# Kernel optimization log

Hardware: AMD Instinct MI355X
Metric: run time of the kernel (lower is better)

Reference implementation:

```python
import jax, jax.numpy as jnp
import numpy as np

B, S, M = 128, 4096, 20
LOG_2PI = float(np.log(2.0 * np.pi))


def setup_inputs() -> dict:
    key = jax.random.key(0)
    k1, k2, k3, k4, k5 = jax.random.split(key, 5)
    xs = jax.random.normal(k1, (B, S, 5), dtype=jnp.float32)
    logits_pred = jax.random.normal(k2, (B, S, M), dtype=jnp.float32)
    mus_pred = jax.random.normal(k3, (B, S, M, 2), dtype=jnp.float32)
    # sigmas are Cholesky entries (l00, l10, l11); diagonal must be positive.
    sigmas_pred = jax.random.uniform(k4, (B, S, M, 3), dtype=jnp.float32) + 0.1
    pen_pred = jax.random.uniform(k5, (B, S, 3), dtype=jnp.float32)
    return {"xs": xs, "logits_pred": logits_pred, "mus_pred": mus_pred,
            "sigmas_pred": sigmas_pred, "pen_pred": pen_pred}


def reference(xs, logits_pred, mus_pred, sigmas_pred, pen_pred):
    # split stroke-5 format: (dx_abs, dy_abs) + 3 pen states
    position_true = xs[..., :2]          # [B,S,2]
    pen_true = xs[..., 2:]               # [B,S,3]

    # relative positions: roll by 1 along seq, first step prev = (0,0)
    position_prev = jnp.concatenate(
        [jnp.zeros_like(position_true[:, :1]), position_true[:, :-1]], axis=1)
    rel = position_true - position_prev  # [B,S,2]

    # closed-form 2D Gaussian log-density with lower-tri Cholesky
    # scale_tril entries (tril_indices(2,2) order): l00, l10, l11
    l00 = sigmas_pred[..., 0]            # [B,S,M]
    l10 = sigmas_pred[..., 1]
    l11 = sigmas_pred[..., 2]
    d = rel[:, :, None, :] - mus_pred    # [B,S,M,2]
    z0 = d[..., 0] / l00
    z1 = (d[..., 1] - l10 * z0) / l11
    comp_logp = (-0.5 * (z0 * z0 + z1 * z1)
                 - LOG_2PI - jnp.log(l00) - jnp.log(l11))  # [B,S,M]

    # mixture log-prob via logsumexp over components
    mix_logp = jax.nn.logsumexp(
        jax.nn.log_softmax(logits_pred, axis=-1) + comp_logp, axis=-1)  # [B,S]
    position_loss = -jnp.sum(mix_logp)

    # pen loss: faithful to source -> CrossEntropyLoss(input=pen_true, target=pen_pred)
    # (soft-target CE, mean reduction over B*S rows)
    logp = jax.nn.log_softmax(pen_true.reshape(-1, 3), axis=-1)
    pen_loss = jnp.mean(-jnp.sum(pen_pred.reshape(-1, 3) * logp, axis=-1))

    return position_loss + pen_loss
```

## Files before the change

### kernel.cpp

```cpp
#include <hip/hip_runtime.h>
#include <math.h>

#define BB 128
#define SS 4096
#define MM 20
#define NPOS (BB * SS)
#define BLOCK 256
#define CHUNK 64
#define CPB 16
#define GRID (NPOS / (CHUNK * CPB))
#define BUF_FLOATS (CHUNK * 120)

__device__ __forceinline__ float fast_rcp(float x) { return __builtin_amdgcn_rcpf(x); }

__device__ __forceinline__ void async_ld16(float* lds, const float* g) {
    __builtin_amdgcn_global_load_lds(
        (const __attribute__((address_space(1))) void*)g,
        (__attribute__((address_space(3))) void*)lds, 16, 0, 0);
}

__device__ __forceinline__ void stage_chunk(
    float* __restrict__ buf, const float* __restrict__ sg,
    const float* __restrict__ mg, const float* __restrict__ lg, int tid)
{
#pragma unroll
    for (int r = 0; r < 7; ++r) {
        int i = tid + r * 256;
        if (i < 960)       async_ld16(buf + i * 4, sg + (size_t)i * 4);
        else if (i < 1600) async_ld16(buf + i * 4, mg + (size_t)(i - 960) * 4);
        else               async_ld16(buf + i * 4, lg + (size_t)(i - 1600) * 4);
    }
    if (tid < 128) {
        int i = 1792 + tid;
        async_ld16(buf + i * 4, lg + (size_t)(i - 1600) * 4);
    }
}

__global__ __launch_bounds__(BLOCK) void sketch_main(
    const float* __restrict__ xs,
    const float* __restrict__ logits,
    const float* __restrict__ mus,
    const float* __restrict__ sigmas,
    const float* __restrict__ pen_pred,
    float* __restrict__ partials)
{
    const float LOG_2PI = 1.8378770664093453f;
    __shared__ float buf[2][BUF_FLOATS];
    __shared__ float red[BLOCK / 64];

    const int tid  = threadIdx.x;
    const int pos  = tid >> 2;
    const int sub  = tid & 3;
    const int lane = tid & 63;
    const int block_base = blockIdx.x * (CHUNK * CPB);

    float acc = 0.0f;

    stage_chunk(buf[0], sigmas + (size_t)block_base * 60,
                mus + (size_t)block_base * 40,
                logits + (size_t)block_base * 20, tid);

    for (int k = 0; k < CPB; ++k) {
        __syncthreads();

        const int base = block_base + (k + 1) * CHUNK;
        if (k + 1 < CPB)
            stage_chunk(buf[(k + 1) & 1], sigmas + (size_t)base * 60,
                        mus + (size_t)base * 40, logits + (size_t)base * 20, tid);

        const float* b = buf[k & 1];
        const int p = block_base + k * CHUNK + pos;
        const float* xp = xs + (size_t)p * 5;

        float rx = 0.0f, ry = 0.0f, penv = 0.0f;
        if (sub == 0) {
            rx = xp[0]; ry = xp[1];
            if ((p & (SS - 1)) != 0) { rx -= xp[-5]; ry -= xp[-4]; }
        } else if (sub == 1) {
            float pt0 = xp[2], pt1 = xp[3], pt2 = xp[4];
            float pm = fmaxf(pt0, fmaxf(pt1, pt2));
            float l3 = pm + __logf(__expf(pt0 - pm) + __expf(pt1 - pm) + __expf(pt2 - pm));
            const float* pp = pen_pred + (size_t)p * 3;
            penv = -(pp[0] * (pt0 - l3) + pp[1] * (pt1 - l3) + pp[2] * (pt2 - l3));
        }
        rx = __shfl(rx, lane & ~3, 64);
        ry = __shfl(ry, lane & ~3, 64);

        const float* S  = b + pos * 60;
        const float* Mu = b + CHUNK * 60 + pos * 40;
        const float* Lg = b + CHUNK * 100 + pos * 20;

        float av[5];
        float sel = 0.0f;
#pragma unroll
        for (int c5 = 0; c5 < 5; ++c5) {
            int c = sub * 5 + c5;
            float l00 = S[c * 3], l10 = S[c * 3 + 1], l11 = S[c * 3 + 2];
            float m0 = Mu[c * 2], m1 = Mu[c * 2 + 1];
            float lgv = Lg[c];
            float z0 = (rx - m0) * fast_rcp(l00);
            float z1 = ((ry - m1) - l10 * z0) * fast_rcp(l11);
            av[c5] = lgv - 0.5f * (z0 * z0 + z1 * z1) - LOG_2PI - __logf(l00 * l11);
            sel += __expf(lgv);
        }
        float mx = fmaxf(fmaxf(fmaxf(av[0], av[1]), fmaxf(av[2], av[3])), av[4]);
        float se = __expf(av[0]-mx) + __expf(av[1]-mx) + __expf(av[2]-mx)
                 + __expf(av[3]-mx) + __expf(av[4]-mx);

#pragma unroll
        for (int off = 1; off <= 2; off <<= 1) {
            float omx = __shfl_xor(mx, off, 64);
            float ose = __shfl_xor(se, off, 64);
            float osl = __shfl_xor(sel, off, 64);
            float nm = fmaxf(mx, omx);
            se = se * __expf(mx - nm) + ose * __expf(omx - nm);
            mx = nm;
            sel += osl;
        }
        if (sub == 0) acc -= (mx + __logf(se)) - __logf(sel);
        acc += penv * (1.0f / (float)NPOS);
    }

#pragma unroll
    for (int off = 32; off > 0; off >>= 1) acc += __shfl_down(acc, off, 64);
    if (lane == 0) red[tid >> 6] = acc;
    __syncthreads();
    if (tid == 0) partials[blockIdx.x] = red[0] + red[1] + red[2] + red[3];
}

__global__ __launch_bounds__(256) void sketch_reduce(
    const float* __restrict__ partials, float* __restrict__ out)
{
    float v = 0.0f;
    for (int i = threadIdx.x; i < GRID; i += 256) v += partials[i];
#pragma unroll
    for (int off = 32; off > 0; off >>= 1) v += __shfl_down(v, off, 64);
    __shared__ float red[4];
    int lane = threadIdx.x & 63, wid = threadIdx.x >> 6;
    if (lane == 0) red[wid] = v;
    __syncthreads();
    if (threadIdx.x == 0)
        out[0] = red[0] + red[1] + red[2] + red[3];
}

extern "C" void kernel_launch(void* const* d_in, const int* in_sizes, int n_in,
                              void* d_out, int out_size, void* d_ws, size_t ws_size,
                              hipStream_t stream) {
    const float* xs       = (const float*)d_in[0];
    const float* logits   = (const float*)d_in[1];
    const float* mus      = (const float*)d_in[2];
    const float* sigmas   = (const float*)d_in[3];
    const float* pen_pred = (const float*)d_in[4];
    float* out = (float*)d_out;
    float* partials = (float*)d_ws;

    sketch_main<<<GRID, BLOCK, 0, stream>>>(xs, logits, mus, sigmas, pen_pred, partials);
    sketch_reduce<<<1, 256, 0, stream>>>(partials, out);
}
```

Measured before the change: 286.4 us.

## Replace async LDS staging with direct per-component global loads and LDS logsumexp

Drops the double-buffered global_load_lds staging of sigmas, mus and logits. Each thread now reads one component's parameters straight from global memory (strided scalar loads), computes its log-density and writes it to LDS, and a second phase does the per-position logsumexp from LDS. Chunks per block go from 16 to 4, so there are four times as many blocks. The change trades explicit prefetch overlap for more blocks and occupancy, at the cost of uncoalesced stride-3 and stride-2 global loads and extra barriers per chunk.

Result: no change. 283.6 us (-1.0%).

```diff
diff --git a/kernel.cpp b/kernel.cpp
--- a/kernel.cpp
+++ b/kernel.cpp
@@ -7,34 +7,10 @@
 #define NPOS (BB * SS)
 #define BLOCK 256
 #define CHUNK 64
-#define CPB 16
+#define CPB 4
 #define GRID (NPOS / (CHUNK * CPB))
-#define BUF_FLOATS (CHUNK * 120)
 
 __device__ __forceinline__ float fast_rcp(float x) { return __builtin_amdgcn_rcpf(x); }
-
-__device__ __forceinline__ void async_ld16(float* lds, const float* g) {
-    __builtin_amdgcn_global_load_lds(
-        (const __attribute__((address_space(1))) void*)g,
-        (__attribute__((address_space(3))) void*)lds, 16, 0, 0);
-}
-
-__device__ __forceinline__ void stage_chunk(
-    float* __restrict__ buf, const float* __restrict__ sg,
-    const float* __restrict__ mg, const float* __restrict__ lg, int tid)
-{
-#pragma unroll
-    for (int r = 0; r < 7; ++r) {
-        int i = tid + r * 256;
-        if (i < 960)       async_ld16(buf + i * 4, sg + (size_t)i * 4);
-        else if (i < 1600) async_ld16(buf + i * 4, mg + (size_t)(i - 960) * 4);
-        else               async_ld16(buf + i * 4, lg + (size_t)(i - 1600) * 4);
-    }
-    if (tid < 128) {
-        int i = 1792 + tid;
-        async_ld16(buf + i * 4, lg + (size_t)(i - 1600) * 4);
-    }
-}
 
 __global__ __launch_bounds__(BLOCK) void sketch_main(
     const float* __restrict__ xs,
@@ -45,67 +21,69 @@
     float* __restrict__ partials)
 {
     const float LOG_2PI = 1.8378770664093453f;
-    __shared__ float buf[2][BUF_FLOATS];
+    __shared__ float avb[CHUNK * MM];
+    __shared__ float lgb[CHUNK * MM];
+    __shared__ float relx[CHUNK], rely[CHUNK];
     __shared__ float red[BLOCK / 64];
 
-    const int tid  = threadIdx.x;
-    const int pos  = tid >> 2;
-    const int sub  = tid & 3;
-    const int lane = tid & 63;
-    const int block_base = blockIdx.x * (CHUNK * CPB);
-
+    const int tid = threadIdx.x;
     float acc = 0.0f;
 
-    stage_chunk(buf[0], sigmas + (size_t)block_base * 60,
-                mus + (size_t)block_base * 40,
-                logits + (size_t)block_base * 20, tid);
+    for (int k = 0; k < CPB; ++k) {
+        const int base = blockIdx.x * (CHUNK * CPB) + k * CHUNK;
 
-    for (int k = 0; k < CPB; ++k) {
+        if (tid < CHUNK) {
+            const int p = base + tid;
+            const float* xp = xs + (size_t)p * 5;
+            float rx = xp[0], ry = xp[1];
+            if ((p & (SS - 1)) != 0) { rx -= xp[-5]; ry -= xp[-4]; }
+            relx[tid] = rx; rely[tid] = ry;
+        } else if (tid < 2 * CHUNK) {
+            const int p = base + (tid - CHUNK);
+            const float* xp = xs + (size_t)p * 5;
+            float pt0 = xp[2], pt1 = xp[3], pt2 = xp[4];
+            float pm = fmaxf(pt0, fmaxf(pt1, pt2));
+            float l3 = pm + __logf(__expf(pt0-pm) + __expf(pt1-pm) + __expf(pt2-pm));
+            const float* pp = pen_pred + (size_t)p * 3;
+            acc -= (pp[0]*(pt0-l3) + pp[1]*(pt1-l3) + pp[2]*(pt2-l3))
+                   * (1.0f / (float)NPOS);
+        }
         __syncthreads();
 
-        const int base = block_base + (k + 1) * CHUNK;
-        if (k + 1 < CPB)
-            stage_chunk(buf[(k + 1) & 1], sigmas + (size_t)base * 60,
-                        mus + (size_t)base * 40, logits + (size_t)base * 20, tid);
+        const float* Sg = sigmas + (size_t)base * 60;
+        const float* Mg = mus    + (size_t)base * 40;
+        const float* Lg = logits + (size_t)base * 20;
 
-        const float* b = buf[k & 1];
-        const int p = block_base + k * CHUNK + pos;
-        const float* xp = xs + (size_t)p * 5;
+        float v00[5], v10[5], v11[5], vm0[5], vm1[5], vlg[5];
+#pragma unroll
+        for (int r = 0; r < 5; ++r) {
+            int c = r * BLOCK + tid;
+            v00[r] = Sg[3*c];  v10[r] = Sg[3*c+1];  v11[r] = Sg[3*c+2];
+            vm0[r] = Mg[2*c];  vm1[r] = Mg[2*c+1];
+            vlg[r] = Lg[c];
+        }
+#pragma unroll
+        for (int r = 0; r < 5; ++r) {
+            int c = r * BLOCK + tid;
+            int pl = c / 20;
+            float rx = relx[pl], ry = rely[pl];
+            float z0 = (rx - vm0[r]) * fast_rcp(v00[r]);
+            float z1 = ((ry - vm1[r]) - v10[r] * z0) * fast_rcp(v11[r]);
+            avb[c] = vlg[r] - 0.5f * (z0*z0 + z1*z1) - LOG_2PI
+                     - __logf(v00[r] * v11[r]);
+            lgb[c] = vlg[r];
+        }
+        __syncthreads();
 
-        float rx = 0.0f, ry = 0.0f, penv = 0.0f;
-        if (sub == 0) {
-            rx = xp[0]; ry = xp[1];
-            if ((p & (SS - 1)) != 0) { rx -= xp[-5]; ry -= xp[-4]; }
-        } else if (sub == 1) {
-            float pt0 = xp[2], pt1 = xp[3], pt2 = xp[4];
-            float pm = fmaxf(pt0, fmaxf(pt1, pt2));
-            float l3 = pm + __logf(__expf(pt0 - pm) + __expf(pt1 - pm) + __expf(pt2 - pm));
-            const float* pp = pen_pred + (size_t)p * 3;
-            penv = -(pp[0] * (pt0 - l3) + pp[1] * (pt1 - l3) + pp[2] * (pt2 - l3));
-        }
-        rx = __shfl(rx, lane & ~3, 64);
-        ry = __shfl(ry, lane & ~3, 64);
-
-        const float* S  = b + pos * 60;
-        const float* Mu = b + CHUNK * 60 + pos * 40;
-        const float* Lg = b + CHUNK * 100 + pos * 20;
-
-        float av[5];
-        float sel = 0.0f;
-#pragma unroll
-        for (int c5 = 0; c5 < 5; ++c5) {
-            int c = sub * 5 + c5;
-            float l00 = S[c * 3], l10 = S[c * 3 + 1], l11 = S[c * 3 + 2];
-            float m0 = Mu[c * 2], m1 = Mu[c * 2 + 1];
-            float lgv = Lg[c];
-            float z0 = (rx - m0) * fast_rcp(l00);
-            float z1 = ((ry - m1) - l10 * z0) * fast_rcp(l11);
-            av[c5] = lgv - 0.5f * (z0 * z0 + z1 * z1) - LOG_2PI - __logf(l00 * l11);
-            sel += __expf(lgv);
-        }
-        float mx = fmaxf(fmaxf(fmaxf(av[0], av[1]), fmaxf(av[2], av[3])), av[4]);
-        float se = __expf(av[0]-mx) + __expf(av[1]-mx) + __expf(av[2]-mx)
-                 + __expf(av[3]-mx) + __expf(av[4]-mx);
+        const int pos = tid >> 2, sub = tid & 3;
+        const float* A = avb + pos * MM + sub * 5;
+        const float* G = lgb + pos * MM + sub * 5;
+        float a0=A[0], a1=A[1], a2=A[2], a3=A[3], a4=A[4];
+        float mx = fmaxf(fmaxf(fmaxf(a0,a1), fmaxf(a2,a3)), a4);
+        float se = __expf(a0-mx)+__expf(a1-mx)+__expf(a2-mx)
+                 + __expf(a3-mx)+__expf(a4-mx);
+        float sel = __expf(G[0])+__expf(G[1])+__expf(G[2])
+                  + __expf(G[3])+__expf(G[4]);
 
 #pragma unroll
         for (int off = 1; off <= 2; off <<= 1) {
@@ -118,12 +96,12 @@
             sel += osl;
         }
         if (sub == 0) acc -= (mx + __logf(se)) - __logf(sel);
-        acc += penv * (1.0f / (float)NPOS);
+        __syncthreads();
     }
 
 #pragma unroll
     for (int off = 32; off > 0; off >>= 1) acc += __shfl_down(acc, off, 64);
-    if (lane == 0) red[tid >> 6] = acc;
+    if ((tid & 63) == 0) red[tid >> 6] = acc;
     __syncthreads();
     if (tid == 0) partials[blockIdx.x] = red[0] + red[1] + red[2] + red[3];
 }
```
